# Kernel tuning notes

Hardware: AMD Instinct MI355X
Metric: run time of the kernel (lower is better)

Reference implementation:

```python
import jax, jax.numpy as jnp
import numpy as np
from functools import lru_cache

SEG_GROUPS = 2          # len(segment_lengths) = len([1024, 2048])
HEAD_DIM = 64
SCALE = HEAD_DIM ** -0.5


@lru_cache(maxsize=None)
def _hilbert_perm(n: int):
    """Replicates _generate_hilbert_indices. For n a perfect power of 4 this is a
    true permutation (and its inverse)."""
    dim = 1
    while dim * dim < n:
        dim *= 2
    idxs = []
    for i in range(min(n, dim * dim)):
        x = y = 0
        s = 1
        t = i
        while s < dim:
            rx = 1 & (t // 2)
            ry = 1 & (t ^ rx)
            if ry == 0:
                if rx == 1:
                    x, y = dim and (s - 1 - y), (s - 1 - x)
                x, y = y, x
            x += s * rx
            y += s * ry
            t //= 4
            s *= 2
        cell = x * dim + y
        if cell < n:
            idxs.append(cell)
    if len(idxs) < n:
        idxs.extend(range(len(idxs), n))
    hil = np.asarray(idxs[:n], dtype=np.int64)
    inv = np.zeros(n, dtype=np.int64)
    inv[hil] = np.arange(n, dtype=np.int64)
    return hil, inv


def setup_inputs() -> dict:
    key = jax.random.key(0)
    k1, k2, k3 = jax.random.split(key, 3)
    shape = (4, 4096, 16, 64)  # [batch, seq_len, num_heads, head_dim]
    return {
        "q": jax.random.normal(k1, shape, dtype=jnp.float32),
        "k": jax.random.normal(k2, shape, dtype=jnp.float32),
        "v": jax.random.normal(k3, shape, dtype=jnp.float32),
    }


def reference(q, k, v):
    """Faithful translation of RingDilatedAttentionHilbertOptimizedFixed.forward
    with is_causal=False, dropout=0, dilation_rates=[1,1].

    Fidelity notes:
    - The torch code matmuls [B, L, h, d] @ [B, L, d, h] WITHOUT moving heads to a
      batch dim, so scores are [B, L, h, h]: per-position head-vs-head attention.
      With dilation_rate=1 this makes the segment loop a pure partition of the
      sequence, so we vectorize over the whole (Hilbert-ordered) sequence.
    - Hilbert gather on q/k/v and inverse scatter on the output are kept.
    """
    B, S, H, D = q.shape
    hil_np, inv_np = _hilbert_perm(S)
    hil = jnp.asarray(hil_np)
    inv = jnp.asarray(inv_np)

    # Hilbert-curve reordering along the sequence axis.
    qo = jnp.take(q, hil, axis=1)
    ko = jnp.take(k, hil, axis=1)
    vo = jnp.take(v, hil, axis=1)

    hg = max(1, H // SEG_GROUPS)  # heads_per_segment
    outs = []
    for g in range(SEG_GROUPS):
        hs, he = g * hg, min(g * hg + hg, H)
        qs, ks, vs = qo[:, :, hs:he], ko[:, :, hs:he], vo[:, :, hs:he]
        # per-position head-vs-head scores: [B, S, hg, hg]
        scores = jnp.einsum("bsid,bsjd->bsij", qs, ks) * SCALE
        attn = jax.nn.softmax(scores, axis=-1)
        attn = jnp.nan_to_num(attn, nan=0.0)
        outs.append(jnp.einsum("bsij,bsjd->bsid", attn, vs))
    out = jnp.concatenate(outs, axis=2)  # heads fully covered: 2 * 8 = 16

    # Inverse Hilbert reordering.
    return jnp.take(out, inv, axis=1)
```

## Files before the change

kernel.cpp:

```cpp
#include <hip/hip_runtime.h>
#include <math.h>


#define HEADS 16
#define DIM 64
#define GSTRIDE 516
#define TSLICE  (2 * GSTRIDE)
#define WSLICE  (2 * TSLICE)
#define WAVES_PER_BLOCK 4

__global__ void __launch_bounds__(256) hilbert_attn_kernel(
    const float* __restrict__ q,
    const float* __restrict__ k,
    const float* __restrict__ v,
    float* __restrict__ out,
    int npos)
{
    __shared__ float lds[WAVES_PER_BLOCK * WSLICE];

    const int t    = threadIdx.x;
    const int wave = t >> 6;
    const int lane = t & 63;
    const long long pos = (long long)blockIdx.x * WAVES_PER_BLOCK + wave;
    if (pos >= npos) return;

    float* kk = lds + wave * WSLICE;
    float* vv = kk + TSLICE;

    const long long gbase = pos * (HEADS * DIM);

    const int i   = lane >> 2;
    const int s   = lane & 3;
    const int grp = i >> 3;

    const float* qp = q + gbase + i * DIM + s * 16;
    float4 q0 = *(const float4*)(qp + 0);
    float4 q1 = *(const float4*)(qp + 4);
    float4 q2 = *(const float4*)(qp + 8);
    float4 q3 = *(const float4*)(qp + 12);

    {
        #pragma unroll
        for (int it = 0; it < 4; ++it) {
            const int sfo = it * 256 + lane * 4;
            const int dfo = sfo + ((it >= 2) ? 4 : 0);
            float4 a = *(const float4*)(k + gbase + sfo);
            float4 b = *(const float4*)(v + gbase + sfo);
            *(float4*)(kk + dfo) = a;
            *(float4*)(vv + dfo) = b;
        }
    }

    const float* kg = kk + grp * GSTRIDE;
    float sc[8];
    #pragma unroll
    for (int j = 0; j < 8; ++j) {
        const float* kr = kg + j * DIM + s * 16;
        float4 k0 = *(const float4*)(kr + 0);
        float4 k1 = *(const float4*)(kr + 4);
        float4 k2 = *(const float4*)(kr + 8);
        float4 k3 = *(const float4*)(kr + 12);
        float a = q0.x*k0.x + q0.y*k0.y + q0.z*k0.z + q0.w*k0.w
                + q1.x*k1.x + q1.y*k1.y + q1.z*k1.z + q1.w*k1.w
                + q2.x*k2.x + q2.y*k2.y + q2.z*k2.z + q2.w*k2.w
                + q3.x*k3.x + q3.y*k3.y + q3.z*k3.z + q3.w*k3.w;
        sc[j] = a;
    }
    #pragma unroll
    for (int j = 0; j < 8; ++j) {
        sc[j] += __shfl_xor(sc[j], 1);
        sc[j] += __shfl_xor(sc[j], 2);
        sc[j] *= 0.125f;
    }

    float m = sc[0];
    #pragma unroll
    for (int j = 1; j < 8; ++j) m = fmaxf(m, sc[j]);
    float sum = 0.f;
    float at[8];
    #pragma unroll
    for (int j = 0; j < 8; ++j) { at[j] = __expf(sc[j] - m); sum += at[j]; }
    const float inv = 1.f / sum;
    #pragma unroll
    for (int j = 0; j < 8; ++j) at[j] *= inv;

    const float* vg = vv + grp * GSTRIDE;
    float4 o0 = make_float4(0,0,0,0), o1 = o0, o2 = o0, o3 = o0;
    #pragma unroll
    for (int j = 0; j < 8; ++j) {
        const float a = at[j];
        const float* vr = vg + j * DIM + s * 16;
        float4 v0 = *(const float4*)(vr + 0);
        float4 v1 = *(const float4*)(vr + 4);
        float4 v2 = *(const float4*)(vr + 8);
        float4 v3 = *(const float4*)(vr + 12);
        o0.x += a*v0.x; o0.y += a*v0.y; o0.z += a*v0.z; o0.w += a*v0.w;
        o1.x += a*v1.x; o1.y += a*v1.y; o1.z += a*v1.z; o1.w += a*v1.w;
        o2.x += a*v2.x; o2.y += a*v2.y; o2.z += a*v2.z; o2.w += a*v2.w;
        o3.x += a*v3.x; o3.y += a*v3.y; o3.z += a*v3.z; o3.w += a*v3.w;
    }

    float* op = out + gbase + i * DIM + s * 16;
    *(float4*)(op + 0)  = o0;
    *(float4*)(op + 4)  = o1;
    *(float4*)(op + 8)  = o2;
    *(float4*)(op + 12) = o3;
}

extern "C" void kernel_launch(void* const* d_in, const int* in_sizes, int n_in,
                              void* d_out, int out_size, void* d_ws, size_t ws_size,
                              hipStream_t stream) {
    const float* q = (const float*)d_in[0];
    const float* k = (const float*)d_in[1];
    const float* v = (const float*)d_in[2];
    float* out = (float*)d_out;

    const int npos = in_sizes[0] / (HEADS * DIM);
    const int blocks = (npos + WAVES_PER_BLOCK - 1) / WAVES_PER_BLOCK;
    hilbert_attn_kernel<<<blocks, 256, 0, stream>>>(q, k, v, out, npos);
}
```

Measured before the change: 210.3 us.

## Software-pipeline per-wave position loop with register double-buffered prefetch

Each wave now handles several positions in a grid-stride loop, issuing global loads for the next position into a second register set while the current one is staged to LDS and computed. Output stores become nontemporal, and the launch shrinks to a quarter of the blocks with a min-blocks launch bound. The aim is to hide global-memory latency in this bandwidth-bound kernel, at the cost of more registers per thread and fewer waves in flight.

```diff
diff --git a/kernel.cpp b/kernel.cpp
--- a/kernel.cpp
+++ b/kernel.cpp
@@ -7,66 +7,62 @@
 #define GSTRIDE 516
 #define TSLICE  (2 * GSTRIDE)
 #define WSLICE  (2 * TSLICE)
-#define WAVES_PER_BLOCK 4
+#define WPB 4
+#define TPW 4
 
-__global__ void __launch_bounds__(256) hilbert_attn_kernel(
-    const float* __restrict__ q,
-    const float* __restrict__ k,
-    const float* __restrict__ v,
-    float* __restrict__ out,
-    int npos)
+typedef float f32x4 __attribute__((ext_vector_type(4)));
+
+__device__ __forceinline__ void issue_loads(
+    const float* __restrict__ q, const float* __restrict__ k,
+    const float* __restrict__ v, long long gbase, int lane,
+    f32x4* qr, f32x4* ks, f32x4* vs)
 {
-    __shared__ float lds[WAVES_PER_BLOCK * WSLICE];
+    const int i = lane >> 2;
+    const int s = lane & 3;
+    const float* qp = q + gbase + i * DIM + s * 16;
+    qr[0] = *(const f32x4*)(qp + 0);
+    qr[1] = *(const f32x4*)(qp + 4);
+    qr[2] = *(const f32x4*)(qp + 8);
+    qr[3] = *(const f32x4*)(qp + 12);
+#pragma unroll
+    for (int it = 0; it < 4; ++it) {
+        const int sfo = it * 256 + lane * 4;
+        ks[it] = *(const f32x4*)(k + gbase + sfo);
+        vs[it] = *(const f32x4*)(v + gbase + sfo);
+    }
+}
 
-    const int t    = threadIdx.x;
-    const int wave = t >> 6;
-    const int lane = t & 63;
-    const long long pos = (long long)blockIdx.x * WAVES_PER_BLOCK + wave;
-    if (pos >= npos) return;
+__device__ __forceinline__ void stage_to_lds(
+    float* kk, float* vv, int lane, const f32x4* ks, const f32x4* vs)
+{
+#pragma unroll
+    for (int it = 0; it < 4; ++it) {
+        const int dfo = it * 256 + lane * 4 + ((it >= 2) ? 4 : 0);
+        *(f32x4*)(kk + dfo) = ks[it];
+        *(f32x4*)(vv + dfo) = vs[it];
+    }
+}
 
-    float* kk = lds + wave * WSLICE;
-    float* vv = kk + TSLICE;
-
-    const long long gbase = pos * (HEADS * DIM);
-
+__device__ __forceinline__ void compute_store(
+    const float* kk, const float* vv, int lane, const f32x4* qr,
+    float* __restrict__ outp)
+{
     const int i   = lane >> 2;
     const int s   = lane & 3;
     const int grp = i >> 3;
 
-    const float* qp = q + gbase + i * DIM + s * 16;
-    float4 q0 = *(const float4*)(qp + 0);
-    float4 q1 = *(const float4*)(qp + 4);
-    float4 q2 = *(const float4*)(qp + 8);
-    float4 q3 = *(const float4*)(qp + 12);
-
-    {
-        #pragma unroll
-        for (int it = 0; it < 4; ++it) {
-            const int sfo = it * 256 + lane * 4;
-            const int dfo = sfo + ((it >= 2) ? 4 : 0);
-            float4 a = *(const float4*)(k + gbase + sfo);
-            float4 b = *(const float4*)(v + gbase + sfo);
-            *(float4*)(kk + dfo) = a;
-            *(float4*)(vv + dfo) = b;
-        }
-    }
-
     const float* kg = kk + grp * GSTRIDE;
     float sc[8];
-    #pragma unroll
+#pragma unroll
     for (int j = 0; j < 8; ++j) {
         const float* kr = kg + j * DIM + s * 16;
-        float4 k0 = *(const float4*)(kr + 0);
-        float4 k1 = *(const float4*)(kr + 4);
-        float4 k2 = *(const float4*)(kr + 8);
-        float4 k3 = *(const float4*)(kr + 12);
-        float a = q0.x*k0.x + q0.y*k0.y + q0.z*k0.z + q0.w*k0.w
-                + q1.x*k1.x + q1.y*k1.y + q1.z*k1.z + q1.w*k1.w
-                + q2.x*k2.x + q2.y*k2.y + q2.z*k2.z + q2.w*k2.w
-                + q3.x*k3.x + q3.y*k3.y + q3.z*k3.z + q3.w*k3.w;
-        sc[j] = a;
+        f32x4 p = qr[0] * *(const f32x4*)(kr + 0)
+                + qr[1] * *(const f32x4*)(kr + 4)
+                + qr[2] * *(const f32x4*)(kr + 8)
+                + qr[3] * *(const f32x4*)(kr + 12);
+        sc[j] = p.x + p.y + p.z + p.w;
     }
-    #pragma unroll
+#pragma unroll
     for (int j = 0; j < 8; ++j) {
         sc[j] += __shfl_xor(sc[j], 1);
         sc[j] += __shfl_xor(sc[j], 2);
@@ -74,37 +70,73 @@
     }
 
     float m = sc[0];
-    #pragma unroll
+#pragma unroll
     for (int j = 1; j < 8; ++j) m = fmaxf(m, sc[j]);
+    float at[8];
     float sum = 0.f;
-    float at[8];
-    #pragma unroll
+#pragma unroll
     for (int j = 0; j < 8; ++j) { at[j] = __expf(sc[j] - m); sum += at[j]; }
     const float inv = 1.f / sum;
-    #pragma unroll
+#pragma unroll
     for (int j = 0; j < 8; ++j) at[j] *= inv;
 
     const float* vg = vv + grp * GSTRIDE;
-    float4 o0 = make_float4(0,0,0,0), o1 = o0, o2 = o0, o3 = o0;
-    #pragma unroll
+    f32x4 o0 = {0.f, 0.f, 0.f, 0.f};
+    f32x4 o1 = o0, o2 = o0, o3 = o0;
+#pragma unroll
     for (int j = 0; j < 8; ++j) {
         const float a = at[j];
         const float* vr = vg + j * DIM + s * 16;
-        float4 v0 = *(const float4*)(vr + 0);
-        float4 v1 = *(const float4*)(vr + 4);
-        float4 v2 = *(const float4*)(vr + 8);
-        float4 v3 = *(const float4*)(vr + 12);
-        o0.x += a*v0.x; o0.y += a*v0.y; o0.z += a*v0.z; o0.w += a*v0.w;
-        o1.x += a*v1.x; o1.y += a*v1.y; o1.z += a*v1.z; o1.w += a*v1.w;
-        o2.x += a*v2.x; o2.y += a*v2.y; o2.z += a*v2.z; o2.w += a*v2.w;
-        o3.x += a*v3.x; o3.y += a*v3.y; o3.z += a*v3.z; o3.w += a*v3.w;
+        o0 += a * *(const f32x4*)(vr + 0);
+        o1 += a * *(const f32x4*)(vr + 4);
+        o2 += a * *(const f32x4*)(vr + 8);
+        o3 += a * *(const f32x4*)(vr + 12);
     }
 
-    float* op = out + gbase + i * DIM + s * 16;
-    *(float4*)(op + 0)  = o0;
-    *(float4*)(op + 4)  = o1;
-    *(float4*)(op + 8)  = o2;
-    *(float4*)(op + 12) = o3;
+    float* op = outp + i * DIM + s * 16;
+    __builtin_nontemporal_store(o0, (f32x4*)(op + 0));
+    __builtin_nontemporal_store(o1, (f32x4*)(op + 4));
+    __builtin_nontemporal_store(o2, (f32x4*)(op + 8));
+    __builtin_nontemporal_store(o3, (f32x4*)(op + 12));
+}
+
+__global__ void __launch_bounds__(256, 4) hilbert_attn_kernel(
+    const float* __restrict__ q,
+    const float* __restrict__ k,
+    const float* __restrict__ v,
+    float* __restrict__ out,
+    int npos)
+{
+    __shared__ float lds[WPB * WSLICE];
+    const int wave = threadIdx.x >> 6;
+    const int lane = threadIdx.x & 63;
+    const long long nw = (long long)gridDim.x * WPB;
+
+    long long t0 = (long long)blockIdx.x * WPB + wave;
+    if (t0 >= npos) return;
+
+    float* kk = lds + wave * WSLICE;
+    float* vv = kk + TSLICE;
+
+    f32x4 qA[4], kA[4], vA[4];
+    f32x4 qB[4], kB[4], vB[4];
+
+    issue_loads(q, k, v, t0 * (HEADS * DIM), lane, qA, kA, vA);
+
+    for (;;) {
+        const long long t1 = t0 + nw;
+        if (t1 < npos) issue_loads(q, k, v, t1 * (HEADS * DIM), lane, qB, kB, vB);
+        stage_to_lds(kk, vv, lane, kA, vA);
+        compute_store(kk, vv, lane, qA, out + t0 * (HEADS * DIM));
+        if (t1 >= npos) return;
+
+        const long long t2 = t1 + nw;
+        if (t2 < npos) issue_loads(q, k, v, t2 * (HEADS * DIM), lane, qA, kA, vA);
+        stage_to_lds(kk, vv, lane, kB, vB);
+        compute_store(kk, vv, lane, qB, out + t1 * (HEADS * DIM));
+        if (t2 >= npos) return;
+        t0 = t2;
+    }
 }
 
 extern "C" void kernel_launch(void* const* d_in, const int* in_sizes, int n_in,
@@ -116,6 +148,6 @@
     float* out = (float*)d_out;
 
     const int npos = in_sizes[0] / (HEADS * DIM);
-    const int blocks = (npos + WAVES_PER_BLOCK - 1) / WAVES_PER_BLOCK;
-    hilbert_attn_kernel<<<blocks, 256, 0, stream>>>(q, k, v, out, npos);
+    const int blocks = (npos + WPB * TPW - 1) / (WPB * TPW);
+    hilbert_attn_kernel<<<blocks, WPB * 64, 0, stream>>>(q, k, v, out, npos);
 }
```

Result: slower. 255.7 us (+21.6%).

## Split work to one wave per head group and widen per-position parallelism

Applied to the files above, without the earlier changes.

Each wave now handles a single 8-head group of one position instead of all 16 heads, doubling the wave count. Each lane covers 8 dims instead of 16, with a three-step shuffle reduction. The K/V staging in shared memory drops the padded group stride, and launch bounds request 8 blocks per CU. This aims to raise occupancy and cut per-thread register use in a memory-bound kernel, at the cost of an extra shuffle step and possible LDS bank conflicts now that the padding is gone.

```diff
diff --git a/kernel.cpp b/kernel.cpp
--- a/kernel.cpp
+++ b/kernel.cpp
@@ -4,107 +4,90 @@
 
 #define HEADS 16
 #define DIM 64
-#define GSTRIDE 516
-#define TSLICE  (2 * GSTRIDE)
-#define WSLICE  (2 * TSLICE)
-#define WAVES_PER_BLOCK 4
+#define GH 8
+#define GFLOATS (GH * DIM)
+#define WSLICE (2 * GFLOATS)
+#define WPB 4
 
-__global__ void __launch_bounds__(256) hilbert_attn_kernel(
+typedef float f32x4 __attribute__((ext_vector_type(4)));
+
+__global__ void __launch_bounds__(256, 8) hilbert_attn_kernel(
     const float* __restrict__ q,
     const float* __restrict__ k,
     const float* __restrict__ v,
     float* __restrict__ out,
     int npos)
 {
-    __shared__ float lds[WAVES_PER_BLOCK * WSLICE];
+    __shared__ float lds[WPB * WSLICE];
+    const int wave = threadIdx.x >> 6;
+    const int lane = threadIdx.x & 63;
 
-    const int t    = threadIdx.x;
-    const int wave = t >> 6;
-    const int lane = t & 63;
-    const long long pos = (long long)blockIdx.x * WAVES_PER_BLOCK + wave;
+    const long long w   = (long long)blockIdx.x * WPB + wave;
+    const long long pos = w >> 1;
+    const int       grp = (int)(w & 1);
     if (pos >= npos) return;
 
     float* kk = lds + wave * WSLICE;
-    float* vv = kk + TSLICE;
+    float* vv = kk + GFLOATS;
 
-    const long long gbase = pos * (HEADS * DIM);
+    const long long gbase = pos * (HEADS * DIM) + (long long)grp * GFLOATS;
 
-    const int i   = lane >> 2;
-    const int s   = lane & 3;
-    const int grp = i >> 3;
+    const int i = lane >> 3;
+    const int s = lane & 7;
 
-    const float* qp = q + gbase + i * DIM + s * 16;
-    float4 q0 = *(const float4*)(qp + 0);
-    float4 q1 = *(const float4*)(qp + 4);
-    float4 q2 = *(const float4*)(qp + 8);
-    float4 q3 = *(const float4*)(qp + 12);
+    const float* qp = q + gbase + i * DIM + s * 8;
+    f32x4 q0 = *(const f32x4*)(qp + 0);
+    f32x4 q1 = *(const f32x4*)(qp + 4);
 
-    {
-        #pragma unroll
-        for (int it = 0; it < 4; ++it) {
-            const int sfo = it * 256 + lane * 4;
-            const int dfo = sfo + ((it >= 2) ? 4 : 0);
-            float4 a = *(const float4*)(k + gbase + sfo);
-            float4 b = *(const float4*)(v + gbase + sfo);
-            *(float4*)(kk + dfo) = a;
-            *(float4*)(vv + dfo) = b;
-        }
+#pragma unroll
+    for (int r = 0; r < 2; ++r) {
+        const int fo = r * 256 + lane * 4;
+        f32x4 a = *(const f32x4*)(k + gbase + fo);
+        f32x4 b = *(const f32x4*)(v + gbase + fo);
+        *(f32x4*)(kk + fo) = a;
+        *(f32x4*)(vv + fo) = b;
     }
 
-    const float* kg = kk + grp * GSTRIDE;
     float sc[8];
-    #pragma unroll
+#pragma unroll
     for (int j = 0; j < 8; ++j) {
-        const float* kr = kg + j * DIM + s * 16;
-        float4 k0 = *(const float4*)(kr + 0);
-        float4 k1 = *(const float4*)(kr + 4);
-        float4 k2 = *(const float4*)(kr + 8);
-        float4 k3 = *(const float4*)(kr + 12);
-        float a = q0.x*k0.x + q0.y*k0.y + q0.z*k0.z + q0.w*k0.w
-                + q1.x*k1.x + q1.y*k1.y + q1.z*k1.z + q1.w*k1.w
-                + q2.x*k2.x + q2.y*k2.y + q2.z*k2.z + q2.w*k2.w
-                + q3.x*k3.x + q3.y*k3.y + q3.z*k3.z + q3.w*k3.w;
-        sc[j] = a;
+        const float* kr = kk + j * DIM + s * 8;
+        f32x4 p = q0 * *(const f32x4*)(kr + 0)
+                + q1 * *(const f32x4*)(kr + 4);
+        sc[j] = p.x + p.y + p.z + p.w;
     }
-    #pragma unroll
+#pragma unroll
     for (int j = 0; j < 8; ++j) {
         sc[j] += __shfl_xor(sc[j], 1);
         sc[j] += __shfl_xor(sc[j], 2);
+        sc[j] += __shfl_xor(sc[j], 4);
         sc[j] *= 0.125f;
     }
 
     float m = sc[0];
-    #pragma unroll
+#pragma unroll
     for (int j = 1; j < 8; ++j) m = fmaxf(m, sc[j]);
+    float at[8];
     float sum = 0.f;
-    float at[8];
-    #pragma unroll
+#pragma unroll
     for (int j = 0; j < 8; ++j) { at[j] = __expf(sc[j] - m); sum += at[j]; }
     const float inv = 1.f / sum;
-    #pragma unroll
+#pragma unroll
     for (int j = 0; j < 8; ++j) at[j] *= inv;
 
-    const float* vg = vv + grp * GSTRIDE;
-    float4 o0 = make_float4(0,0,0,0), o1 = o0, o2 = o0, o3 = o0;
-    #pragma unroll
+    f32x4 o0 = {0.f, 0.f, 0.f, 0.f};
+    f32x4 o1 = o0;
+#pragma unroll
     for (int j = 0; j < 8; ++j) {
         const float a = at[j];
-        const float* vr = vg + j * DIM + s * 16;
-        float4 v0 = *(const float4*)(vr + 0);
-        float4 v1 = *(const float4*)(vr + 4);
-        float4 v2 = *(const float4*)(vr + 8);
-        float4 v3 = *(const float4*)(vr + 12);
-        o0.x += a*v0.x; o0.y += a*v0.y; o0.z += a*v0.z; o0.w += a*v0.w;
-        o1.x += a*v1.x; o1.y += a*v1.y; o1.z += a*v1.z; o1.w += a*v1.w;
-        o2.x += a*v2.x; o2.y += a*v2.y; o2.z += a*v2.z; o2.w += a*v2.w;
-        o3.x += a*v3.x; o3.y += a*v3.y; o3.z += a*v3.z; o3.w += a*v3.w;
+        const float* vr = vv + j * DIM + s * 8;
+        o0 += a * *(const f32x4*)(vr + 0);
+        o1 += a * *(const f32x4*)(vr + 4);
     }
 
-    float* op = out + gbase + i * DIM + s * 16;
-    *(float4*)(op + 0)  = o0;
-    *(float4*)(op + 4)  = o1;
-    *(float4*)(op + 8)  = o2;
-    *(float4*)(op + 12) = o3;
+    float* op = out + gbase + i * DIM + s * 8;
+    *(f32x4*)(op + 0) = o0;
+    *(f32x4*)(op + 4) = o1;
 }
 
 extern "C" void kernel_launch(void* const* d_in, const int* in_sizes, int n_in,
@@ -116,6 +99,7 @@
     float* out = (float*)d_out;
 
     const int npos = in_sizes[0] / (HEADS * DIM);
-    const int blocks = (npos + WAVES_PER_BLOCK - 1) / WAVES_PER_BLOCK;
-    hilbert_attn_kernel<<<blocks, 256, 0, stream>>>(q, k, v, out, npos);
+    const long long nwaves = 2LL * npos;
+    const int blocks = (int)((nwaves + WPB - 1) / WPB);
+    hilbert_attn_kernel<<<blocks, WPB * 64, 0, stream>>>(q, k, v, out, npos);
 }
```

Result: no change. 211.6 us (+0.6%).
